# Performance work log

Measured on AMD Instinct MI355X. Metric: run time of the kernel, lower is better.

The kernel has to match this reference:

```python
import jax, jax.numpy as jnp
import numpy as np

B, T, S, D = 8, 32, 256, 1024


def setup_inputs() -> dict:
    key = jax.random.key(0)
    ks = jax.random.split(key, 10)
    scale = 1.0 / np.sqrt(D)
    return {
        "source1": jax.random.normal(ks[0], (B, T, D), jnp.float32),
        "source2": jax.random.normal(ks[1], (B, T, D), jnp.float32),
        "memory_bank": jax.random.normal(ks[2], (B, S, D), jnp.float32),
        "source_masks1": jnp.ones((B, T), jnp.float32),
        "source_masks2": jnp.ones((B, T), jnp.float32),
        "W_q1": jax.random.normal(ks[3], (D, D), jnp.float32) * scale,
        "b_q1": jnp.zeros((D,), jnp.float32),
        "W_q2": jax.random.normal(ks[4], (D, D), jnp.float32) * scale,
        "b_q2": jnp.zeros((D,), jnp.float32),
        "W_cate": jax.random.normal(ks[5], (2, 2 * D), jnp.float32) * scale,
        "b_cate": jnp.zeros((2,), jnp.float32),
        "W_v": jax.random.normal(ks[6], (D, D), jnp.float32) * scale,
    }


def reference(source1, source2, memory_bank, source_masks1, source_masks2,
              W_q1, b_q1, W_q2, b_q2, W_cate, b_cate, W_v):
    Bq, Tq, Dd = source1.shape
    # accumulate(): running prefix-mean over the segment axis, then mask.
    denom = jnp.arange(1, Tq + 1, dtype=source1.dtype)[None, :, None]
    s1 = (jnp.cumsum(source1, axis=1) / denom) * source_masks1[:, :, None]
    s2 = (jnp.cumsum(source2, axis=1) / denom) * source_masks2[:, :, None]
    # score(): gated attention scoring.
    q1 = s1 @ W_q1.T + b_q1  # [B,T,D]
    q2 = s2 @ W_q2.T + b_q2  # [B,T,D]
    # tanh gate broadcast over all (tgt, src) pairs -> [B,T,S,D]
    g = jnp.tanh(q1[:, :, None, :] + q2[:, :, None, :] + memory_bank[:, None, :, :])
    # sum_j (g @ W_v.T)[..., j] == g @ sum_j W_v[j, :]
    w_colsum = jnp.sum(W_v, axis=0)              # [D]
    sum_gate = g @ w_colsum                       # [B,T,S]
    # linear_cate(concat([h_s, sum_gate*h_s])) split into two halves
    pa = memory_bank @ W_cate[:, :Dd].T           # [B,S,2]
    pb = memory_bank @ W_cate[:, Dd:].T           # [B,S,2]
    out = pa[:, None, :, :] + sum_gate[..., None] * pb[:, None, :, :] + b_cate
    return out  # [B,T,S,2]
```

## Files before the change

### kernel.cpp

```cpp
#include <hip/hip_runtime.h>
#include <hip/hip_bf16.h>

#define Bb 8
#define Tt 32
#define Ss 256
#define Dd 1024
#define SCALE 2.885390081777927f

typedef short short8 __attribute__((ext_vector_type(8)));
typedef float floatx4 __attribute__((ext_vector_type(4)));

__device__ __forceinline__ unsigned short bf16b(float x) {
    __hip_bfloat16 h = __float2bfloat16(x);
    return *(unsigned short*)&h;
}

__device__ __forceinline__ float dot4(float4 a, float4 b) {
    return a.x * b.x + a.y * b.y + a.z * b.z + a.w * b.w;
}

__device__ __forceinline__ float sigm_term(float q, float m, float w, float acc) {
    float e = __builtin_amdgcn_exp2f(q + m);
    return fmaf(w, __builtin_amdgcn_rcpf(e + 1.f), acc);
}

__global__ __launch_bounds__(256) void prep_kernel(
        const float* __restrict__ src1, const float* __restrict__ src2,
        const float* __restrict__ m1, const float* __restrict__ m2,
        const float* __restrict__ W1, const float* __restrict__ W2,
        const float* __restrict__ Wv,
        unsigned short* __restrict__ W1b, unsigned short* __restrict__ W2b,
        unsigned short* __restrict__ s1b, unsigned short* __restrict__ s2b,
        float* __restrict__ part) {
    const int blk = blockIdx.x, tid = threadIdx.x;
    if (blk < 1024) {
        const int idx = blk * 256 + tid;
        float4 a = ((const float4*)W1)[idx];
        float4 b = ((const float4*)W2)[idx];
        ushort4 oa = { bf16b(a.x), bf16b(a.y), bf16b(a.z), bf16b(a.w) };
        ushort4 ob = { bf16b(b.x), bf16b(b.y), bf16b(b.z), bf16b(b.w) };
        ((ushort4*)W1b)[idx] = oa;
        ((ushort4*)W2b)[idx] = ob;
    } else if (blk < 1088) {
        const int bb = blk - 1024;
        const int db = bb & 3, jc = bb >> 2;
        const int d = db * 256 + tid;
        float a = 0.f;
        const int j0 = jc * 64;
        for (int j = 0; j < 64; j++)
            a += Wv[(size_t)(j0 + j) * Dd + d];
        part[jc * Dd + d] = a;
    } else {
        const int idx = (blk - 1088) * 256 + tid;
        const int srcsel = idx >> 13;
        const int bd = idx & 8191;
        const int b = bd >> 10, d = bd & 1023;
        const float* sp = srcsel ? src2 : src1;
        const float* mp = srcsel ? m2 : m1;
        unsigned short* op = srcsel ? s2b : s1b;
        float a = 0.f;
        for (int t = 0; t < Tt; t++) {
            a += sp[(size_t)(b * Tt + t) * Dd + d];
            float inv = __builtin_amdgcn_rcpf((float)(t + 1));
            op[(size_t)(b * Tt + t) * Dd + d] = bf16b(a * inv * mp[b * Tt + t]);
        }
    }
}

__global__ __launch_bounds__(64) void gemm_kernel(
        const unsigned short* __restrict__ s1b, const unsigned short* __restrict__ s2b,
        const unsigned short* __restrict__ W1b, const unsigned short* __restrict__ W2b,
        const float* __restrict__ bq1, const float* __restrict__ bq2,
        const float* __restrict__ part, const float* __restrict__ mem,
        const float* __restrict__ Wc,
        float* __restrict__ qp, float* __restrict__ wsum,
        float* __restrict__ pab) {
    const int blk = blockIdx.x;
    const int lane = threadIdx.x;
    if (blk >= 528) {
        const int bs = blk - 528;
        const float4* mrow = (const float4*)mem + (size_t)bs * 256;
        const float4* Wc4 = (const float4*)Wc;
        float a0 = 0.f, a1 = 0.f, b0 = 0.f, b1 = 0.f;
        #pragma unroll
        for (int j = 0; j < 4; j++) {
            const int idx = j * 64 + lane;
            float4 m_ = mrow[idx];
            a0 += dot4(m_, Wc4[idx]);
            b0 += dot4(m_, Wc4[256 + idx]);
            a1 += dot4(m_, Wc4[512 + idx]);
            b1 += dot4(m_, Wc4[768 + idx]);
        }
        #pragma unroll
        for (int o = 32; o > 0; o >>= 1) {
            a0 += __shfl_xor(a0, o);
            a1 += __shfl_xor(a1, o);
            b0 += __shfl_xor(b0, o);
            b1 += __shfl_xor(b1, o);
        }
        if (lane == 0) {
            float4 r = { a0, a1, b0, b1 };
            ((float4*)pab)[bs] = r;
        }
        return;
    }
    if (blk >= 512) {
        const int d = (blk - 512) * 64 + lane;
        float a = 0.f;
        #pragma unroll
        for (int jc = 0; jc < 16; jc++)
            a += part[jc * Dd + d];
        wsum[d] = a;
        return;
    }
    const int m0 = (blk & 15) * 16;
    const int n0 = (blk >> 4) * 32;
    const int lm = lane & 15;
    const int quad = lane >> 4;

    floatx4 acc0 = {0.f, 0.f, 0.f, 0.f};
    floatx4 acc1 = {0.f, 0.f, 0.f, 0.f};
    const unsigned short* a1p = s1b + (size_t)(m0 + lm) * Dd;
    const unsigned short* a2p = s2b + (size_t)(m0 + lm) * Dd;
    const unsigned short* b1a = W1b + (size_t)(n0 + lm) * Dd;
    const unsigned short* b1b = W1b + (size_t)(n0 + 16 + lm) * Dd;
    const unsigned short* b2a = W2b + (size_t)(n0 + lm) * Dd;
    const unsigned short* b2b = W2b + (size_t)(n0 + 16 + lm) * Dd;

    #pragma unroll 2
    for (int k0 = 0; k0 < Dd; k0 += 32) {
        const int off = k0 + quad * 8;
        short8 a1 = *(const short8*)(a1p + off);
        short8 a2 = *(const short8*)(a2p + off);
        short8 vb1a = *(const short8*)(b1a + off);
        short8 vb2a = *(const short8*)(b2a + off);
        short8 vb1b = *(const short8*)(b1b + off);
        short8 vb2b = *(const short8*)(b2b + off);
        acc0 = __builtin_amdgcn_mfma_f32_16x16x32_bf16(a1, vb1a, acc0, 0, 0, 0);
        acc1 = __builtin_amdgcn_mfma_f32_16x16x32_bf16(a1, vb1b, acc1, 0, 0, 0);
        acc0 = __builtin_amdgcn_mfma_f32_16x16x32_bf16(a2, vb2a, acc0, 0, 0, 0);
        acc1 = __builtin_amdgcn_mfma_f32_16x16x32_bf16(a2, vb2b, acc1, 0, 0, 0);
    }

    const int na = n0 + lm, nb = n0 + 16 + lm;
    const float biasa = bq1[na] + bq2[na];
    const float biasb = bq1[nb] + bq2[nb];
    #pragma unroll
    for (int r = 0; r < 4; r++) {
        const int m = m0 + quad * 4 + r;
        qp[(size_t)m * Dd + na] = SCALE * (acc0[r] + biasa);
        qp[(size_t)m * Dd + nb] = SCALE * (acc1[r] + biasb);
    }
}

__global__ __launch_bounds__(256) void out_kernel(
        const float* __restrict__ qp, const float* __restrict__ mem,
        const float* __restrict__ wsum, const float* __restrict__ pab,
        const float* __restrict__ bc, float* __restrict__ out) {
    const int wave = threadIdx.x >> 6;
    const int lane = threadIdx.x & 63;
    const int gid = blockIdx.x * 4 + wave;
    const int b = gid >> 9;
    const int r = gid & 511;
    const int tq = r >> 6, sq = r & 63;
    const int t0 = tq * 4, s0 = sq * 4;
    const int bs0 = b * Ss + s0;

    const float4* mem4 = (const float4*)mem;
    const float4* q4 = (const float4*)qp;
    const float4* wsum4 = (const float4*)wsum;

    float4 wv[4];
    float Wl = 0.f;
    #pragma unroll
    for (int j = 0; j < 4; j++) {
        wv[j] = wsum4[j * 64 + lane];
        Wl += wv[j].x + wv[j].y + wv[j].z + wv[j].w;
    }
    #pragma unroll
    for (int o = 32; o > 0; o >>= 1) Wl += __shfl_xor(Wl, o);

    const float bc0 = bc[0], bc1 = bc[1];
    float C0[4], C1[4], D0[4], D1[4];
    #pragma unroll
    for (int si = 0; si < 4; si++) {
        float4 pv = ((const float4*)pab)[bs0 + si];
        C0[si] = pv.x + Wl * pv.z + bc0;
        C1[si] = pv.y + Wl * pv.w + bc1;
        D0[si] = 2.f * pv.z;
        D1[si] = 2.f * pv.w;
    }

    float p[4][4];
    #pragma unroll
    for (int ti = 0; ti < 4; ti++)
        #pragma unroll
        for (int si = 0; si < 4; si++) p[ti][si] = 0.f;

    #pragma unroll
    for (int j = 0; j < 4; j++) {
        const int idx = j * 64 + lane;
        float4 mj[4], qj[4];
        #pragma unroll
        for (int si = 0; si < 4; si++) {
            float4 m_ = mem4[(size_t)(bs0 + si) * 256 + idx];
            mj[si].x = m_.x * SCALE; mj[si].y = m_.y * SCALE;
            mj[si].z = m_.z * SCALE; mj[si].w = m_.w * SCALE;
        }
        #pragma unroll
        for (int ti = 0; ti < 4; ti++)
            qj[ti] = q4[(size_t)(b * Tt + t0 + ti) * 256 + idx];
        const float4 w_ = wv[j];
        #pragma unroll
        for (int ti = 0; ti < 4; ti++) {
            #pragma unroll
            for (int si = 0; si < 4; si++) {
                float acc = p[ti][si];
                acc = sigm_term(qj[ti].x, mj[si].x, w_.x, acc);
                acc = sigm_term(qj[ti].y, mj[si].y, w_.y, acc);
                acc = sigm_term(qj[ti].z, mj[si].z, w_.z, acc);
                acc = sigm_term(qj[ti].w, mj[si].w, w_.w, acc);
                p[ti][si] = acc;
            }
        }
    }

    #pragma unroll
    for (int ti = 0; ti < 4; ti++)
        #pragma unroll
        for (int si = 0; si < 4; si++) {
            float v = p[ti][si];
            #pragma unroll
            for (int o = 32; o > 0; o >>= 1) v += __shfl_xor(v, o);
            p[ti][si] = v;
        }

    if (lane == 0) {
        #pragma unroll
        for (int ti = 0; ti < 4; ti++) {
            const size_t rowo = ((size_t)(b * Tt + t0 + ti) * Ss + s0) * 2;
            #pragma unroll
            for (int si = 0; si < 4; si++) {
                float2 o2 = { C0[si] - D0[si] * p[ti][si],
                              C1[si] - D1[si] * p[ti][si] };
                *(float2*)(out + rowo + si * 2) = o2;
            }
        }
    }
}

extern "C" void kernel_launch(void* const* d_in, const int* in_sizes, int n_in,
                              void* d_out, int out_size, void* d_ws, size_t ws_size,
                              hipStream_t stream) {
    const float* src1 = (const float*)d_in[0];
    const float* src2 = (const float*)d_in[1];
    const float* mem  = (const float*)d_in[2];
    const float* m1   = (const float*)d_in[3];
    const float* m2   = (const float*)d_in[4];
    const float* Wq1  = (const float*)d_in[5];
    const float* bq1  = (const float*)d_in[6];
    const float* Wq2  = (const float*)d_in[7];
    const float* bq2  = (const float*)d_in[8];
    const float* Wc   = (const float*)d_in[9];
    const float* bc   = (const float*)d_in[10];
    const float* Wv   = (const float*)d_in[11];
    float* out = (float*)d_out;

    char* ws = (char*)d_ws;
    unsigned short* s1b = (unsigned short*)(ws);
    unsigned short* s2b = (unsigned short*)(ws + (512u << 10));
    unsigned short* W1b = (unsigned short*)(ws + (1u << 20));
    unsigned short* W2b = (unsigned short*)(ws + (3u << 20));
    float* qp   = (float*)(ws + (5u << 20));
    float* wsum = (float*)(ws + (6u << 20));
    float* part = (float*)(ws + (6u << 20) + 4096);
    float* pab  = (float*)(ws + (6u << 20) + 4096 + 65536);

    prep_kernel<<<1152, 256, 0, stream>>>(src1, src2, m1, m2, Wq1, Wq2, Wv,
                                          W1b, W2b, s1b, s2b, part);
    gemm_kernel<<<2576, 64, 0, stream>>>(s1b, s2b, W1b, W2b, bq1, bq2, part,
                                         mem, Wc, qp, wsum, pab);
    out_kernel<<<1024, 256, 0, stream>>>(qp, mem, wsum, pab, bc, out);
}
```

Measured before the change: 125.0 us.

## Fuse prep, GEMM and output stages into one cooperative kernel with grid syncs

Replaces the three back-to-back kernel launches with a single cooperative kernel of 1024 blocks that runs the bf16 conversion and prefix-mean, the MFMA projection GEMM, and the tanh-gate output stage, separated by grid-wide syncs. The aim is to remove inter-kernel launch gaps and drain time. In exchange, work is redistributed over fewer waves: the GEMM phase uses only one in eight waves, and occupancy is capped by the co-residency requirement. It falls back to the old three-kernel path if the occupancy check or the cooperative launch fails.

Result: no change. 126.8 us (+1.4%).

```diff
diff --git a/kernel.cpp b/kernel.cpp
--- a/kernel.cpp
+++ b/kernel.cpp
@@ -1,5 +1,8 @@
 #include <hip/hip_runtime.h>
 #include <hip/hip_bf16.h>
+#include <hip/hip_cooperative_groups.h>
+
+namespace cg = cooperative_groups;
 
 #define Bb 8
 #define Tt 32
@@ -22,6 +25,231 @@
 __device__ __forceinline__ float sigm_term(float q, float m, float w, float acc) {
     float e = __builtin_amdgcn_exp2f(q + m);
     return fmaf(w, __builtin_amdgcn_rcpf(e + 1.f), acc);
+}
+
+__global__ __launch_bounds__(256, 4) void fused_kernel(
+        const float* __restrict__ src1, const float* __restrict__ src2,
+        const float* __restrict__ mem,
+        const float* __restrict__ m1, const float* __restrict__ m2,
+        const float* __restrict__ W1, const float* __restrict__ bq1,
+        const float* __restrict__ W2, const float* __restrict__ bq2,
+        const float* __restrict__ Wc, const float* __restrict__ bc,
+        const float* __restrict__ Wv,
+        unsigned short* __restrict__ s1b, unsigned short* __restrict__ s2b,
+        unsigned short* __restrict__ W1b, unsigned short* __restrict__ W2b,
+        float* __restrict__ qp, float* __restrict__ wsum,
+        float* __restrict__ part, float* __restrict__ pab,
+        float* __restrict__ out) {
+    cg::grid_group grid = cg::this_grid();
+    const int gthread = blockIdx.x * 256 + threadIdx.x;
+    const int wave = gthread >> 6;
+    const int lane = gthread & 63;
+
+    {
+        const int idx = gthread;
+        float4 a = ((const float4*)W1)[idx];
+        float4 b = ((const float4*)W2)[idx];
+        ushort4 oa = { bf16b(a.x), bf16b(a.y), bf16b(a.z), bf16b(a.w) };
+        ushort4 ob = { bf16b(b.x), bf16b(b.y), bf16b(b.z), bf16b(b.w) };
+        ((ushort4*)W1b)[idx] = oa;
+        ((ushort4*)W2b)[idx] = ob;
+    }
+    if ((wave & 1) == 0) {
+        const int bs = wave >> 1;
+        const float4* mrow = (const float4*)mem + (size_t)bs * 256;
+        const float4* Wc4 = (const float4*)Wc;
+        float a0 = 0.f, a1 = 0.f, b0 = 0.f, b1 = 0.f;
+        #pragma unroll
+        for (int j = 0; j < 4; j++) {
+            const int idx = j * 64 + lane;
+            float4 m_ = mrow[idx];
+            a0 += dot4(m_, Wc4[idx]);
+            b0 += dot4(m_, Wc4[256 + idx]);
+            a1 += dot4(m_, Wc4[512 + idx]);
+            b1 += dot4(m_, Wc4[768 + idx]);
+        }
+        #pragma unroll
+        for (int o = 32; o > 0; o >>= 1) {
+            a0 += __shfl_xor(a0, o);
+            a1 += __shfl_xor(a1, o);
+            b0 += __shfl_xor(b0, o);
+            b1 += __shfl_xor(b1, o);
+        }
+        if (lane == 0) {
+            float4 r = { a0, a1, b0, b1 };
+            ((float4*)pab)[bs] = r;
+        }
+    } else if ((wave & 15) == 1) {
+        const int idx = (wave >> 4) * 64 + lane;
+        const int srcsel = idx >> 13;
+        const int bd = idx & 8191;
+        const int b = bd >> 10, d = bd & 1023;
+        const float* sp = srcsel ? src2 : src1;
+        const float* mp = srcsel ? m2 : m1;
+        unsigned short* op = srcsel ? s2b : s1b;
+        float a = 0.f;
+        for (int t = 0; t < Tt; t++) {
+            a += sp[(size_t)(b * Tt + t) * Dd + d];
+            float inv = __builtin_amdgcn_rcpf((float)(t + 1));
+            op[(size_t)(b * Tt + t) * Dd + d] = bf16b(a * inv * mp[b * Tt + t]);
+        }
+    } else if ((wave & 15) == 3) {
+        const int i = (wave >> 4) * 64 + lane;
+        const int d = i & 1023, jc = i >> 10;
+        const int j0 = jc * 64;
+        float a = 0.f;
+        for (int j = 0; j < 64; j++)
+            a += Wv[(size_t)(j0 + j) * Dd + d];
+        part[jc * Dd + d] = a;
+    }
+
+    __threadfence();
+    grid.sync();
+    __threadfence();
+
+    if ((wave & 7) == 0) {
+        const int tile = wave >> 3;
+        const int m0 = (tile & 15) * 16;
+        const int n0 = (tile >> 4) * 32;
+        const int lm = lane & 15;
+        const int quad = lane >> 4;
+
+        floatx4 acc0 = {0.f, 0.f, 0.f, 0.f};
+        floatx4 acc1 = {0.f, 0.f, 0.f, 0.f};
+        const unsigned short* a1p = s1b + (size_t)(m0 + lm) * Dd;
+        const unsigned short* a2p = s2b + (size_t)(m0 + lm) * Dd;
+        const unsigned short* b1a = W1b + (size_t)(n0 + lm) * Dd;
+        const unsigned short* b1b = W1b + (size_t)(n0 + 16 + lm) * Dd;
+        const unsigned short* b2a = W2b + (size_t)(n0 + lm) * Dd;
+        const unsigned short* b2b = W2b + (size_t)(n0 + 16 + lm) * Dd;
+
+        #pragma unroll 2
+        for (int k0 = 0; k0 < Dd; k0 += 32) {
+            const int off = k0 + quad * 8;
+            short8 a1 = *(const short8*)(a1p + off);
+            short8 a2 = *(const short8*)(a2p + off);
+            short8 vb1a = *(const short8*)(b1a + off);
+            short8 vb2a = *(const short8*)(b2a + off);
+            short8 vb1b = *(const short8*)(b1b + off);
+            short8 vb2b = *(const short8*)(b2b + off);
+            acc0 = __builtin_amdgcn_mfma_f32_16x16x32_bf16(a1, vb1a, acc0, 0, 0, 0);
+            acc1 = __builtin_amdgcn_mfma_f32_16x16x32_bf16(a1, vb1b, acc1, 0, 0, 0);
+            acc0 = __builtin_amdgcn_mfma_f32_16x16x32_bf16(a2, vb2a, acc0, 0, 0, 0);
+            acc1 = __builtin_amdgcn_mfma_f32_16x16x32_bf16(a2, vb2b, acc1, 0, 0, 0);
+        }
+
+        const int na = n0 + lm, nb = n0 + 16 + lm;
+        const float biasa = bq1[na] + bq2[na];
+        const float biasb = bq1[nb] + bq2[nb];
+        #pragma unroll
+        for (int r = 0; r < 4; r++) {
+            const int m = m0 + quad * 4 + r;
+            qp[(size_t)m * Dd + na] = SCALE * (acc0[r] + biasa);
+            qp[(size_t)m * Dd + nb] = SCALE * (acc1[r] + biasb);
+        }
+    } else if ((wave & 7) == 4 && (wave >> 3) < 16) {
+        const int d = (wave >> 3) * 64 + lane;
+        float a = 0.f;
+        #pragma unroll
+        for (int jc = 0; jc < 16; jc++)
+            a += part[jc * Dd + d];
+        wsum[d] = a;
+    }
+
+    __threadfence();
+    grid.sync();
+    __threadfence();
+
+    {
+        const int gid = wave;
+        const int b = gid >> 9;
+        const int r = gid & 511;
+        const int tq = r >> 6, sq = r & 63;
+        const int t0 = tq * 4, s0 = sq * 4;
+        const int bs0 = b * Ss + s0;
+
+        const float4* mem4 = (const float4*)mem;
+        const float4* q4 = (const float4*)qp;
+        const float4* wsum4 = (const float4*)wsum;
+
+        float4 wv[4];
+        float Wl = 0.f;
+        #pragma unroll
+        for (int j = 0; j < 4; j++) {
+            wv[j] = wsum4[j * 64 + lane];
+            Wl += wv[j].x + wv[j].y + wv[j].z + wv[j].w;
+        }
+        #pragma unroll
+        for (int o = 32; o > 0; o >>= 1) Wl += __shfl_xor(Wl, o);
+
+        const float bc0 = bc[0], bc1 = bc[1];
+        float C0[4], C1[4], D0[4], D1[4];
+        #pragma unroll
+        for (int si = 0; si < 4; si++) {
+            float4 pv = ((const float4*)pab)[bs0 + si];
+            C0[si] = pv.x + Wl * pv.z + bc0;
+            C1[si] = pv.y + Wl * pv.w + bc1;
+            D0[si] = 2.f * pv.z;
+            D1[si] = 2.f * pv.w;
+        }
+
+        float p[4][4];
+        #pragma unroll
+        for (int ti = 0; ti < 4; ti++)
+            #pragma unroll
+            for (int si = 0; si < 4; si++) p[ti][si] = 0.f;
+
+        #pragma unroll
+        for (int j = 0; j < 4; j++) {
+            const int idx = j * 64 + lane;
+            float4 mj[4], qj[4];
+            #pragma unroll
+            for (int si = 0; si < 4; si++) {
+                float4 m_ = mem4[(size_t)(bs0 + si) * 256 + idx];
+                mj[si].x = m_.x * SCALE; mj[si].y = m_.y * SCALE;
+                mj[si].z = m_.z * SCALE; mj[si].w = m_.w * SCALE;
+            }
+            #pragma unroll
+            for (int ti = 0; ti < 4; ti++)
+                qj[ti] = q4[(size_t)(b * Tt + t0 + ti) * 256 + idx];
+            const float4 w_ = wv[j];
+            #pragma unroll
+            for (int ti = 0; ti < 4; ti++) {
+                #pragma unroll
+                for (int si = 0; si < 4; si++) {
+                    float acc = p[ti][si];
+                    acc = sigm_term(qj[ti].x, mj[si].x, w_.x, acc);
+                    acc = sigm_term(qj[ti].y, mj[si].y, w_.y, acc);
+                    acc = sigm_term(qj[ti].z, mj[si].z, w_.z, acc);
+                    acc = sigm_term(qj[ti].w, mj[si].w, w_.w, acc);
+                    p[ti][si] = acc;
+                }
+            }
+        }
+
+        #pragma unroll
+        for (int ti = 0; ti < 4; ti++)
+            #pragma unroll
+            for (int si = 0; si < 4; si++) {
+                float v = p[ti][si];
+                #pragma unroll
+                for (int o = 32; o > 0; o >>= 1) v += __shfl_xor(v, o);
+                p[ti][si] = v;
+            }
+
+        if (lane == 0) {
+            #pragma unroll
+            for (int ti = 0; ti < 4; ti++) {
+                const size_t rowo = ((size_t)(b * Tt + t0 + ti) * Ss + s0) * 2;
+                #pragma unroll
+                for (int si = 0; si < 4; si++) {
+                    float2 o2 = { C0[si] - D0[si] * p[ti][si],
+                                  C1[si] - D1[si] * p[ti][si] };
+                    *(float2*)(out + rowo + si * 2) = o2;
+                }
+            }
+        }
+    }
 }
 
 __global__ __launch_bounds__(256) void prep_kernel(
@@ -276,6 +504,33 @@
     float* part = (float*)(ws + (6u << 20) + 4096);
     float* pab  = (float*)(ws + (6u << 20) + 4096 + 65536);
 
+    static int s_mode = 0;
+    if (s_mode == 0) {
+        int nb = 0;
+        if (hipOccupancyMaxActiveBlocksPerMultiprocessor(
+                &nb, (const void*)fused_kernel, 256, 0) != hipSuccess) nb = 0;
+        int dev = 0;
+        if (hipGetDevice(&dev) != hipSuccess) dev = 0;
+        int cu = 0;
+        if (hipDeviceGetAttribute(&cu, hipDeviceAttributeMultiprocessorCount,
+                                  dev) != hipSuccess) cu = 0;
+        s_mode = (nb > 0 && cu > 0 && nb * cu >= 1024) ? 1 : 2;
+    }
+
+    if (s_mode == 1) {
+        void* args[] = { (void*)&src1, (void*)&src2, (void*)&mem,
+                         (void*)&m1, (void*)&m2,
+                         (void*)&Wq1, (void*)&bq1, (void*)&Wq2, (void*)&bq2,
+                         (void*)&Wc, (void*)&bc, (void*)&Wv,
+                         (void*)&s1b, (void*)&s2b, (void*)&W1b, (void*)&W2b,
+                         (void*)&qp, (void*)&wsum, (void*)&part, (void*)&pab,
+                         (void*)&out };
+        hipError_t e = hipLaunchCooperativeKernel(
+            (const void*)fused_kernel, dim3(1024), dim3(256), args, 0, stream);
+        if (e == hipSuccess) return;
+        s_mode = 2;
+    }
+
     prep_kernel<<<1152, 256, 0, stream>>>(src1, src2, m1, m2, Wq1, Wq2, Wv,
                                           W1b, W2b, s1b, s2b, part);
     gemm_kernel<<<2576, 64, 0, stream>>>(s1b, s2b, W1b, W2b, bq1, bq2, part,
```

## Factor exp2 of sum into precomputed exponentials and stage memory rows in LDS

Applied to the files above, without the earlier changes.

Uses exp2(q+m) = exp2(q)*exp2(m). The GEMM epilogue now stores exp2 of the scaled query, and the pab pass (moved into prep_kernel) stores exp2 of the scaled memory bank into a workspace buffer. The inner loop of out_kernel then does a multiply instead of a transcendental per term. out_kernel is remapped so each block shares four memory rows across 16 targets, loaded once into shared memory. This costs an extra write and read of a B×S×D float buffer, and large arguments can overflow exp2 where the sum itself would not.

Measured after the change: 119.6 us (median of 2 runs). 1.05x faster.

```diff
diff --git a/kernel.cpp b/kernel.cpp
--- a/kernel.cpp
+++ b/kernel.cpp
@@ -19,8 +19,8 @@
     return a.x * b.x + a.y * b.y + a.z * b.z + a.w * b.w;
 }
 
-__device__ __forceinline__ float sigm_term(float q, float m, float w, float acc) {
-    float e = __builtin_amdgcn_exp2f(q + m);
+__device__ __forceinline__ float sig2(float eqv, float emv, float w, float acc) {
+    float e = eqv * emv;
     return fmaf(w, __builtin_amdgcn_rcpf(e + 1.f), acc);
 }
 
@@ -28,10 +28,12 @@
         const float* __restrict__ src1, const float* __restrict__ src2,
         const float* __restrict__ m1, const float* __restrict__ m2,
         const float* __restrict__ W1, const float* __restrict__ W2,
-        const float* __restrict__ Wv,
+        const float* __restrict__ Wv, const float* __restrict__ mem,
+        const float* __restrict__ Wc,
         unsigned short* __restrict__ W1b, unsigned short* __restrict__ W2b,
         unsigned short* __restrict__ s1b, unsigned short* __restrict__ s2b,
-        float* __restrict__ part) {
+        float* __restrict__ part, float* __restrict__ pab,
+        float* __restrict__ em) {
     const int blk = blockIdx.x, tid = threadIdx.x;
     if (blk < 1024) {
         const int idx = blk * 256 + tid;
@@ -50,7 +52,7 @@
         for (int j = 0; j < 64; j++)
             a += Wv[(size_t)(j0 + j) * Dd + d];
         part[jc * Dd + d] = a;
-    } else {
+    } else if (blk < 1152) {
         const int idx = (blk - 1088) * 256 + tid;
         const int srcsel = idx >> 13;
         const int bd = idx & 8191;
@@ -64,22 +66,11 @@
             float inv = __builtin_amdgcn_rcpf((float)(t + 1));
             op[(size_t)(b * Tt + t) * Dd + d] = bf16b(a * inv * mp[b * Tt + t]);
         }
-    }
-}
-
-__global__ __launch_bounds__(64) void gemm_kernel(
-        const unsigned short* __restrict__ s1b, const unsigned short* __restrict__ s2b,
-        const unsigned short* __restrict__ W1b, const unsigned short* __restrict__ W2b,
-        const float* __restrict__ bq1, const float* __restrict__ bq2,
-        const float* __restrict__ part, const float* __restrict__ mem,
-        const float* __restrict__ Wc,
-        float* __restrict__ qp, float* __restrict__ wsum,
-        float* __restrict__ pab) {
-    const int blk = blockIdx.x;
-    const int lane = threadIdx.x;
-    if (blk >= 528) {
-        const int bs = blk - 528;
+    } else {
+        const int lane = tid & 63;
+        const int bs = (blk - 1152) * 4 + (tid >> 6);
         const float4* mrow = (const float4*)mem + (size_t)bs * 256;
+        float4* emr = (float4*)em + (size_t)bs * 256;
         const float4* Wc4 = (const float4*)Wc;
         float a0 = 0.f, a1 = 0.f, b0 = 0.f, b1 = 0.f;
         #pragma unroll
@@ -90,6 +81,11 @@
             b0 += dot4(m_, Wc4[256 + idx]);
             a1 += dot4(m_, Wc4[512 + idx]);
             b1 += dot4(m_, Wc4[768 + idx]);
+            float4 e4 = { __builtin_amdgcn_exp2f(SCALE * m_.x),
+                          __builtin_amdgcn_exp2f(SCALE * m_.y),
+                          __builtin_amdgcn_exp2f(SCALE * m_.z),
+                          __builtin_amdgcn_exp2f(SCALE * m_.w) };
+            emr[idx] = e4;
         }
         #pragma unroll
         for (int o = 32; o > 0; o >>= 1) {
@@ -102,8 +98,17 @@
             float4 r = { a0, a1, b0, b1 };
             ((float4*)pab)[bs] = r;
         }
-        return;
-    }
+    }
+}
+
+__global__ __launch_bounds__(64) void gemm_kernel(
+        const unsigned short* __restrict__ s1b, const unsigned short* __restrict__ s2b,
+        const unsigned short* __restrict__ W1b, const unsigned short* __restrict__ W2b,
+        const float* __restrict__ bq1, const float* __restrict__ bq2,
+        const float* __restrict__ part,
+        float* __restrict__ qp, float* __restrict__ wsum) {
+    const int blk = blockIdx.x;
+    const int lane = threadIdx.x;
     if (blk >= 512) {
         const int d = (blk - 512) * 64 + lane;
         float a = 0.f;
@@ -148,26 +153,34 @@
     #pragma unroll
     for (int r = 0; r < 4; r++) {
         const int m = m0 + quad * 4 + r;
-        qp[(size_t)m * Dd + na] = SCALE * (acc0[r] + biasa);
-        qp[(size_t)m * Dd + nb] = SCALE * (acc1[r] + biasb);
+        qp[(size_t)m * Dd + na] = __builtin_amdgcn_exp2f(SCALE * (acc0[r] + biasa));
+        qp[(size_t)m * Dd + nb] = __builtin_amdgcn_exp2f(SCALE * (acc1[r] + biasb));
     }
 }
 
 __global__ __launch_bounds__(256) void out_kernel(
-        const float* __restrict__ qp, const float* __restrict__ mem,
+        const float* __restrict__ eq, const float* __restrict__ em,
         const float* __restrict__ wsum, const float* __restrict__ pab,
         const float* __restrict__ bc, float* __restrict__ out) {
-    const int wave = threadIdx.x >> 6;
-    const int lane = threadIdx.x & 63;
-    const int gid = blockIdx.x * 4 + wave;
-    const int b = gid >> 9;
-    const int r = gid & 511;
-    const int tq = r >> 6, sq = r & 63;
-    const int t0 = tq * 4, s0 = sq * 4;
+    __shared__ float em_s[4 * 1024];
+    const int tid = threadIdx.x;
+    const int wave = tid >> 6;
+    const int lane = tid & 63;
+    const int blk = blockIdx.x;
+    const int sq = blk & 63, tg = (blk >> 6) & 1, b = blk >> 7;
+    const int s0 = sq * 4;
+    const int t0 = tg * 16 + wave * 4;
     const int bs0 = b * Ss + s0;
 
-    const float4* mem4 = (const float4*)mem;
-    const float4* q4 = (const float4*)qp;
+    {
+        const float4* eg = (const float4*)em + (size_t)(bs0 + wave) * 256;
+        float4* es = (float4*)em_s + wave * 256;
+        #pragma unroll
+        for (int k = 0; k < 4; k++)
+            es[(tid & 63) + 64 * k] = eg[(tid & 63) + 64 * k];
+    }
+
+    const float4* q4 = (const float4*)eq;
     const float4* wsum4 = (const float4*)wsum;
 
     float4 wv[4];
@@ -197,16 +210,15 @@
         #pragma unroll
         for (int si = 0; si < 4; si++) p[ti][si] = 0.f;
 
+    __syncthreads();
+
     #pragma unroll
     for (int j = 0; j < 4; j++) {
         const int idx = j * 64 + lane;
-        float4 mj[4], qj[4];
-        #pragma unroll
-        for (int si = 0; si < 4; si++) {
-            float4 m_ = mem4[(size_t)(bs0 + si) * 256 + idx];
-            mj[si].x = m_.x * SCALE; mj[si].y = m_.y * SCALE;
-            mj[si].z = m_.z * SCALE; mj[si].w = m_.w * SCALE;
-        }
+        float4 emj[4], qj[4];
+        #pragma unroll
+        for (int si = 0; si < 4; si++)
+            emj[si] = ((const float4*)em_s)[si * 256 + idx];
         #pragma unroll
         for (int ti = 0; ti < 4; ti++)
             qj[ti] = q4[(size_t)(b * Tt + t0 + ti) * 256 + idx];
@@ -216,10 +228,10 @@
             #pragma unroll
             for (int si = 0; si < 4; si++) {
                 float acc = p[ti][si];
-                acc = sigm_term(qj[ti].x, mj[si].x, w_.x, acc);
-                acc = sigm_term(qj[ti].y, mj[si].y, w_.y, acc);
-                acc = sigm_term(qj[ti].z, mj[si].z, w_.z, acc);
-                acc = sigm_term(qj[ti].w, mj[si].w, w_.w, acc);
+                acc = sig2(qj[ti].x, emj[si].x, w_.x, acc);
+                acc = sig2(qj[ti].y, emj[si].y, w_.y, acc);
+                acc = sig2(qj[ti].z, emj[si].z, w_.z, acc);
+                acc = sig2(qj[ti].w, emj[si].w, w_.w, acc);
                 p[ti][si] = acc;
             }
         }
@@ -275,10 +287,12 @@
     float* wsum = (float*)(ws + (6u << 20));
     float* part = (float*)(ws + (6u << 20) + 4096);
     float* pab  = (float*)(ws + (6u << 20) + 4096 + 65536);
-
-    prep_kernel<<<1152, 256, 0, stream>>>(src1, src2, m1, m2, Wq1, Wq2, Wv,
-                                          W1b, W2b, s1b, s2b, part);
-    gemm_kernel<<<2576, 64, 0, stream>>>(s1b, s2b, W1b, W2b, bq1, bq2, part,
-                                         mem, Wc, qp, wsum, pab);
-    out_kernel<<<1024, 256, 0, stream>>>(qp, mem, wsum, pab, bc, out);
-}
+    float* em   = (float*)(ws + (7u << 20));
+
+    prep_kernel<<<1664, 256, 0, stream>>>(src1, src2, m1, m2, Wq1, Wq2, Wv,
+                                          mem, Wc, W1b, W2b, s1b, s2b,
+                                          part, pab, em);
+    gemm_kernel<<<528, 64, 0, stream>>>(s1b, s2b, W1b, W2b, bq1, bq2, part,
+                                        qp, wsum);
+    out_kernel<<<1024, 256, 0, stream>>>(qp, em, wsum, pab, bc, out);
+}
```
